# Kernel tuning notes

Hardware: AMD Instinct MI355X
Metric: run time of the kernel (lower is better)

## Reference

```python
import jax, jax.numpy as jnp
import numpy as np
import math

V, D, H, NH, LE, LD = 32000, 256, 1024, 8, 2, 2
B, T = 4, 512


def qlinear(x, W, b):
    # x: [..., Din, 4]; W: [4, Dout, Din] (r,i,j,k); b: [Dout, 4] or None
    r, i, j, k = x[..., 0], x[..., 1], x[..., 2], x[..., 3]
    Wr, Wi, Wj, Wk = W[0], W[1], W[2], W[3]
    f = lambda a, M: jnp.einsum('...d,od->...o', a, M)
    ro = f(r, Wr) - f(i, Wi) - f(j, Wj) - f(k, Wk)
    io = f(r, Wi) + f(i, Wr) + f(j, Wk) - f(k, Wj)
    jo = f(r, Wj) - f(i, Wk) + f(j, Wr) + f(k, Wi)
    ko = f(r, Wk) + f(i, Wj) - f(j, Wi) + f(k, Wr)
    out = jnp.stack([ro, io, jo, ko], axis=-1)
    return out + b if b is not None else out


def modrelu(x, bias):
    # x: [..., F, 4]; bias: [F]
    norm = jnp.linalg.norm(x, axis=-1)
    scale = jax.nn.relu(norm + bias) / (norm + 1e-6)
    return x * scale[..., None]


def qnorm(x, g, beta):
    # normalize each quaternion (last dim of size 4) to unit norm
    n = jnp.sqrt(jnp.sum(x * x, axis=-1, keepdims=True) + 1e-6)
    return g * (x / n) + beta


def qattn(q, k, v, W, b, mask, nh):
    # W: [4(proj q,k,v,out), 4(comp), D, D]; b: [4, D, 4]
    def split(x):
        Bq, Tq, Dq, _ = x.shape
        return x.reshape(Bq, Tq, nh, Dq // nh, 4).transpose(0, 2, 1, 3, 4)
    qh = split(qlinear(q, W[0], b[0]))
    kh = split(qlinear(k, W[1], b[1]))
    vh = split(qlinear(v, W[2], b[2]))
    hd = qh.shape[3]
    s = jnp.einsum('bhqfd,bhkfd->bhqk', qh, kh) / math.sqrt(hd * 4)
    if mask is not None:
        s = jnp.where(mask[:, None] == 0, -jnp.inf, s)
    w = jax.nn.softmax(s, axis=-1)
    o = jnp.einsum('bhqk,bhkfd->bhqfd', w, vh)
    Bq, h, Tq, f, _ = o.shape
    o = o.transpose(0, 2, 1, 3, 4).reshape(Bq, Tq, h * f, 4)
    return qlinear(o, W[3], b[3])


def qff(x, W1, b1, mbias, W2, b2):
    return qlinear(modrelu(qlinear(x, W1, b1), mbias), W2, b2)


def qembed(ids, emb):
    d = emb.shape[-1]
    scale = 1.0 / 10000.0 ** (jnp.arange(d, dtype=jnp.float32) / d)
    r = emb[0][ids]
    i = emb[1][ids] * scale
    j = emb[2][ids] * scale
    k = emb[3][ids] * scale
    n = jnp.sqrt(r * r + i * i + j * j + k * k + 1e-6)
    return jnp.stack([r / n, i / n, j / n, k / n], axis=-1)


def rope(x):
    t, d = x.shape[1], x.shape[2]
    inv = 1.0 / 10000.0 ** (jnp.arange(0, d, 2, dtype=jnp.float32) / d)
    fr = jnp.arange(t, dtype=jnp.float32)[:, None] * inv[None, :]
    ang = jnp.concatenate([jnp.sin(fr), jnp.cos(fr)], axis=-1)  # [T, D]
    return x * ang[None, :, :, None]


def setup_inputs():
    key = jax.random.key(0)
    ks = jax.random.split(key, 12)
    n = lambda k, s: jax.random.normal(k, s, jnp.float32) * 0.02
    src = jax.random.randint(ks[0], (B, T), 0, V)
    tgt = jax.random.randint(ks[1], (B, T), 0, V)
    tgt_mask = jnp.broadcast_to(jnp.tril(jnp.ones((T, T), jnp.int32)), (B, T, T))
    return dict(
        src=src, tgt=tgt, tgt_mask=tgt_mask,
        emb=n(ks[2], (4, V, D)),
        enc_attn_W=n(ks[3], (LE, 4, 4, D, D)), enc_attn_b=jnp.zeros((LE, 4, D, 4)),
        enc_norm_g=jnp.ones((LE, 2, D, 4)), enc_norm_b=jnp.zeros((LE, 2, D, 4)),
        enc_ff_W1=n(ks[4], (LE, 4, H, D)), enc_ff_b1=jnp.zeros((LE, H, 4)),
        enc_ff_mod=jnp.zeros((LE, H)),
        enc_ff_W2=n(ks[5], (LE, 4, D, H)), enc_ff_b2=jnp.zeros((LE, D, 4)),
        dec_sa_W=n(ks[6], (LD, 4, 4, D, D)), dec_sa_b=jnp.zeros((LD, 4, D, 4)),
        dec_ca_W=n(ks[7], (LD, 4, 4, D, D)), dec_ca_b=jnp.zeros((LD, 4, D, 4)),
        dec_norm_g=jnp.ones((LD, 3, D, 4)), dec_norm_b=jnp.zeros((LD, 3, D, 4)),
        dec_ff_W1=n(ks[8], (LD, 4, H, D)), dec_ff_b1=jnp.zeros((LD, H, 4)),
        dec_ff_mod=jnp.zeros((LD, H)),
        dec_ff_W2=n(ks[9], (LD, 4, D, H)), dec_ff_b2=jnp.zeros((LD, D, 4)),
        fc_W=n(ks[10], (V, D)), fc_b=jnp.zeros((V,)),
    )


def reference(src, tgt, tgt_mask, emb,
              enc_attn_W, enc_attn_b, enc_norm_g, enc_norm_b,
              enc_ff_W1, enc_ff_b1, enc_ff_mod, enc_ff_W2, enc_ff_b2,
              dec_sa_W, dec_sa_b, dec_ca_W, dec_ca_b, dec_norm_g, dec_norm_b,
              dec_ff_W1, dec_ff_b1, dec_ff_mod, dec_ff_W2, dec_ff_b2,
              fc_W, fc_b):
    x_src = rope(qembed(src, emb))
    x_tgt = rope(qembed(tgt, emb))
    # encoder stack
    m = x_src
    for l in range(LE):
        m = qnorm(m + qattn(m, m, m, enc_attn_W[l], enc_attn_b[l], None, NH), enc_norm_g[l, 0], enc_norm_b[l, 0])
        m = qnorm(m + qff(m, enc_ff_W1[l], enc_ff_b1[l], enc_ff_mod[l], enc_ff_W2[l], enc_ff_b2[l]), enc_norm_g[l, 1], enc_norm_b[l, 1])
    # decoder stack
    x = x_tgt
    for l in range(LD):
        x = qnorm(x + qattn(x, x, x, dec_sa_W[l], dec_sa_b[l], tgt_mask, NH), dec_norm_g[l, 0], dec_norm_b[l, 0])
        x = qnorm(x + qattn(x, m, m, dec_ca_W[l], dec_ca_b[l], None, NH), dec_norm_g[l, 1], dec_norm_b[l, 1])
        x = qnorm(x + qff(x, dec_ff_W1[l], dec_ff_b1[l], dec_ff_mod[l], dec_ff_W2[l], dec_ff_b2[l]), dec_norm_g[l, 2], dec_norm_b[l, 2])
    real = jnp.linalg.norm(x, axis=-1)  # QuaternionToReal('norm') -> [B, T, D]
    logits = jnp.einsum('btd,vd->btv', real, fc_W) + fc_b
    return logits
```

## Files before the change

### kernel.cpp

```cpp
#include <hip/hip_runtime.h>
#include <math.h>

#define B 4
#define T 512
#define D 256
#define H 1024
#define NH 8
#define V 32000
#define BT (B*T)
#define LE 2
#define LD 2
#define DIM 1024

typedef __attribute__((ext_vector_type(8))) short s16x8;
typedef __attribute__((ext_vector_type(4))) float f32x4;
typedef __attribute__((address_space(3))) void lds_void;
typedef const __attribute__((address_space(1))) void g_void;

__device__ __forceinline__ ushort f2bf(float x) {
  uint u = __float_as_uint(x);
  return (ushort)((u + 0x7fffu + ((u >> 16) & 1u)) >> 16);
}
__device__ __forceinline__ float bf2f(ushort u) {
  return __uint_as_float(((uint)u) << 16);
}

#define QSCALE 0.08838834764831845f

#define A_CNT  1572864
#define F_CNT  2097152
#define FC_CNT 2048000
#define EMB_CNT (2 * BT * 256)
#define MEGA_TOT (A_CNT + F_CNT + FC_CNT + EMB_CNT)
#define WSTEP  1048576
#define FFW    4194304

__device__ __forceinline__ void qexpand_write(
    const float* __restrict__ src, ushort* __restrict__ dst,
    int o, int d, int Din, int P) {
  float w0 = src[(size_t)o * Din + d];
  float w1 = src[P + (size_t)o * Din + d];
  float w2 = src[2 * (size_t)P + (size_t)o * Din + d];
  float w3 = src[3 * (size_t)P + (size_t)o * Din + d];
  int K4 = Din * 4;
  size_t rbase = (size_t)(o * 4) * K4 + d * 4;
  *(ushort4*)(dst + rbase)          = make_ushort4(f2bf(w0), f2bf(-w1), f2bf(-w2), f2bf(-w3));
  *(ushort4*)(dst + rbase + K4)     = make_ushort4(f2bf(w1), f2bf(w0),  f2bf(w3),  f2bf(-w2));
  *(ushort4*)(dst + rbase + 2 * K4) = make_ushort4(f2bf(w2), f2bf(-w3), f2bf(w0),  f2bf(w1));
  *(ushort4*)(dst + rbase + 3 * K4) = make_ushort4(f2bf(w3), f2bf(w2),  f2bf(-w1), f2bf(w0));
}

__global__ __launch_bounds__(256) void mega_expand_kernel(
    const float* __restrict__ encA, const float* __restrict__ decSA,
    const float* __restrict__ decCA,
    const float* __restrict__ eW1, const float* __restrict__ eW2,
    const float* __restrict__ dW1, const float* __restrict__ dW2,
    const float* __restrict__ fcW,
    ushort* __restrict__ WA, ushort* __restrict__ WF, ushort* __restrict__ Wfc,
    const int* __restrict__ srcIds, const int* __restrict__ tgtIds,
    const float* __restrict__ emb,
    float* __restrict__ xsrc, ushort* __restrict__ xbfs,
    float* __restrict__ xtgt, ushort* __restrict__ xbft) {
  int gid = blockIdx.x * 256 + threadIdx.x;
  if (gid < A_CNT) {
    int u = gid >> 18;
    int p = (gid >> 16) & 3;
    int rem = gid & 65535;
    int o = rem >> 8, d = rem & 255;
    const float* base = (u < 2) ? encA + (size_t)u * 1048576
                      : (u < 4) ? decSA + (size_t)(u - 2) * 1048576
                                : decCA + (size_t)(u - 4) * 1048576;
    qexpand_write(base + (size_t)p * 262144,
                  WA + ((size_t)u * 4 + p) * WSTEP, o, d, 256, 65536);
  } else if (gid < A_CNT + F_CNT) {
    int idx = gid - A_CNT;
    int layer = idx >> 19;
    int w12 = (idx >> 18) & 1;
    int rem = idx & 262143;
    const float* w1b = (layer < 2) ? eW1 + (size_t)layer * 1048576
                                   : dW1 + (size_t)(layer - 2) * 1048576;
    const float* w2b = (layer < 2) ? eW2 + (size_t)layer * 1048576
                                   : dW2 + (size_t)(layer - 2) * 1048576;
    ushort* dst = WF + (size_t)layer * 2 * FFW + (size_t)w12 * FFW;
    if (w12 == 0) {
      int o = rem >> 8, d = rem & 255;
      qexpand_write(w1b, dst, o, d, 256, 262144);
    } else {
      int o = rem >> 10, d = rem & 1023;
      qexpand_write(w2b, dst, o, d, 1024, 262144);
    }
  } else if (gid < A_CNT + F_CNT + FC_CNT) {
    int idx = gid - A_CNT - F_CNT;
    float4 v = ((const float4*)fcW)[idx];
    ((ushort4*)Wfc)[idx] = make_ushort4(f2bf(v.x), f2bf(v.y), f2bf(v.z), f2bf(v.w));
  } else if (gid < MEGA_TOT) {
    int idx = gid - A_CNT - F_CNT - FC_CNT;
    int g = idx >> 8, d = idx & 255;
    int isTgt = g >= BT;
    int bt = isTgt ? g - BT : g;
    int id = isTgt ? tgtIds[bt] : srcIds[bt];
    float* out = isTgt ? xtgt : xsrc;
    ushort* outbf = isTgt ? xbft : xbfs;
    int t = bt % T;
    size_t VD = (size_t)V * D;
    float scale = powf(10000.f, -(float)d / (float)D);
    float r = emb[(size_t)id * D + d];
    float i = emb[VD + (size_t)id * D + d] * scale;
    float j = emb[2 * VD + (size_t)id * D + d] * scale;
    float k = emb[3 * VD + (size_t)id * D + d] * scale;
    float n = sqrtf(r * r + i * i + j * j + k * k + 1e-6f);
    float ang;
    if (d < D / 2) {
      float inv = powf(10000.f, -(float)(2 * d) / (float)D);
      ang = sinf((float)t * inv);
    } else {
      float inv = powf(10000.f, -(float)(2 * (d - D / 2)) / (float)D);
      ang = cosf((float)t * inv);
    }
    float s = ang / n;
    size_t base = (size_t)bt * DIM + d * 4;
    float4 q = make_float4(r * s, i * s, j * s, k * s);
    *(float4*)(out + base) = q;
    *(ushort4*)(outbf + base) = make_ushort4(f2bf(q.x), f2bf(q.y), f2bf(q.z), f2bf(q.w));
  }
}

struct GP {
  const ushort* A; const ushort* Aalt; int altStart;
  const ushort* Bt; const float* bias; void* Cv;
  ushort* qo; ushort* ko; ushort* vo;
  const float* modb;
};

template <int OMODE, int TM>
__global__ __launch_bounds__(256, 4) void gemm_bf16_kernel(
    GP u0, GP u1, int nunits, int nsplit, int N, int K) {
  __shared__ ushort As[2][TM * 32];
  __shared__ ushort Bs[2][128 * 32];
  const int tid = threadIdx.x;
  const int w = tid >> 6, l = tid & 63;
  const int nwg = gridDim.x;
  const int qq = nwg >> 3, rr = nwg & 7;
  const int xcd = blockIdx.x & 7, pos = blockIdx.x >> 3;
  const int wg = (xcd < rr ? xcd * (qq + 1) : rr * (qq + 1) + (xcd - rr) * qq) + pos;
  const int uwg = nwg / (nunits * nsplit);
  const int idx = wg / uwg;
  const int unit = idx / nsplit;
  const int split = idx % nsplit;
  const int wgl = wg % uwg;
  GP U = unit ? u1 : u0;
  const int Ksub = K / nsplit;
  const int kbase = split * Ksub;
  const int nbx = N >> 7;
  const int nby = uwg / nbx;
  const int m0 = (wgl % nby) * TM, n0 = (wgl / nby) * 128;
  const ushort* Ap = (U.altStart && n0 >= U.altStart) ? U.Aalt : U.A;
  const ushort* Btp = U.Bt;
  const int lr = l & 15, lg = l >> 4;
  constexpr int NR = (TM == 128) ? 4 : 2;
  const int wm = (TM == 128) ? (w >> 1) : 0;
  const int wn = (TM == 128) ? (w & 1) : w;
  const int wcol = wn * (NR * 16);
  f32x4 acc[4][NR] = {};
  const int NT = Ksub >> 5;

  auto stage = [&](int t, int buf) {
    int k0 = kbase + (t << 5);
#pragma unroll
    for (int s = 0; s < TM / 64; ++s) {
      int fb = (w * (TM / 64) + s) * 1024;
      int f = fb + l * 16;
      int row = f >> 6, cb = (f & 63) >> 1;
      __builtin_amdgcn_global_load_lds(
          (g_void*)(Ap + (size_t)(m0 + row) * K + k0 + cb),
          (lds_void*)((char*)&As[buf][0] + fb), 16, 0, 0);
    }
#pragma unroll
    for (int s = 0; s < 2; ++s) {
      int fb = (w * 2 + s) * 1024;
      int f = fb + l * 16;
      int row = f >> 6, cb = (f & 63) >> 1;
      __builtin_amdgcn_global_load_lds(
          (g_void*)(Btp + (size_t)(n0 + row) * K + k0 + cb),
          (lds_void*)((char*)&Bs[buf][0] + fb), 16, 0, 0);
    }
  };
  auto compute = [&](int buf) {
    s16x8 af[4], bfr[NR];
#pragma unroll
    for (int mi = 0; mi < 4; ++mi)
      af[mi] = *(const s16x8*)(&As[buf][0] + (wm * 64 + mi * 16 + lr) * 32 + lg * 8);
#pragma unroll
    for (int ni = 0; ni < NR; ++ni)
      bfr[ni] = *(const s16x8*)(&Bs[buf][0] + (wcol + ni * 16 + lr) * 32 + lg * 8);
    __builtin_amdgcn_s_setprio(1);
#pragma unroll
    for (int mi = 0; mi < 4; ++mi)
#pragma unroll
      for (int ni = 0; ni < NR; ++ni)
        acc[mi][ni] = __builtin_amdgcn_mfma_f32_16x16x32_bf16(af[mi], bfr[ni], acc[mi][ni], 0, 0, 0);
    __builtin_amdgcn_s_setprio(0);
  };

  stage(0, 0);
  __syncthreads();
  int cur = 0;
  for (int t = 0; t < NT; ++t) {
    if (t + 1 < NT) stage(t + 1, cur ^ 1);
    compute(cur);
    __syncthreads();
    cur ^= 1;
  }

#pragma unroll
  for (int mi = 0; mi < 4; ++mi) {
#pragma unroll
    for (int ni = 0; ni < NR; ++ni) {
      int row = m0 + wm * 64 + mi * 16 + lg * 4;
      int col = n0 + wcol + ni * 16 + lr;
      f32x4 v = acc[mi][ni];
      if constexpr (OMODE == 0) {
        float bv = U.bias ? U.bias[col] : 0.f;
        float* C = (float*)U.Cv;
#pragma unroll
        for (int r = 0; r < 4; ++r)
          C[(size_t)(row + r) * N + col] = v[r] + bv;
      } else if constexpr (OMODE == 3) {
        float bv = U.bias[col];
        if (col < 2048) {
          ushort* dst = (col < DIM) ? U.qo : U.ko;
          float sc = (col < DIM) ? QSCALE : 1.f;
          int c = col & (DIM - 1);
#pragma unroll
          for (int r = 0; r < 4; ++r)
            dst[(size_t)(row + r) * DIM + c] = f2bf((v[r] + bv) * sc);
        } else {
          int c = col - 2048;
          ushort4 o4 = make_ushort4(f2bf(v[0] + bv), f2bf(v[1] + bv),
                                    f2bf(v[2] + bv), f2bf(v[3] + bv));
          *(ushort4*)&U.vo[((size_t)((row >> 9) << 10) + c) * T + (row & 511)] = o4;
        }
      } else if constexpr (OMODE == 5) {
        float bv = U.bias[col];
        float mb = U.modb[col >> 2];
        ushort* C = (ushort*)U.Cv;
#pragma unroll
        for (int r = 0; r < 4; ++r) {
          float val = v[r] + bv;
          float sq = val * val;
          sq += __shfl_xor(sq, 1);
          sq += __shfl_xor(sq, 2);
          float norm = sqrtf(sq);
          float scale = fmaxf(norm + mb, 0.f) / (norm + 1e-6f);
          C[(size_t)(row + r) * N + col] = f2bf(val * scale);
        }
      } else {
        ushort* P = (ushort*)U.Cv + (size_t)split * BT * N;
#pragma unroll
        for (int r = 0; r < 4; ++r)
          P[(size_t)(row + r) * N + col] = f2bf(v[r]);
      }
    }
  }
}

struct MP {
  const ushort* P; const float* bias;
  float* xres; ushort* xbf;
  const float* gg; const float* bb; ushort* realo;
};

__global__ __launch_bounds__(256) void merge_qnorm_kernel(MP m0, MP m1) {
  int blk = blockIdx.x;
  MP M = (blk >= BT) ? m1 : m0;
  int row = (blk >= BT) ? blk - BT : blk;
  int c4 = threadIdx.x << 2;
  size_t base = (size_t)row * DIM + c4;
  float a0 = 0.f, a1 = 0.f, a2 = 0.f, a3 = 0.f;
#pragma unroll
  for (int sp = 0; sp < 4; ++sp) {
    ushort4 p = *(const ushort4*)(M.P + (size_t)sp * BT * DIM + base);
    a0 += bf2f(p.x); a1 += bf2f(p.y); a2 += bf2f(p.z); a3 += bf2f(p.w);
  }
  float4 xv = *(float4*)(M.xres + base);
  float v0 = a0 + M.bias[c4 + 0] + xv.x;
  float v1 = a1 + M.bias[c4 + 1] + xv.y;
  float v2 = a2 + M.bias[c4 + 2] + xv.z;
  float v3 = a3 + M.bias[c4 + 3] + xv.w;
  float invn = rsqrtf(v0 * v0 + v1 * v1 + v2 * v2 + v3 * v3 + 1e-6f);
  float r0 = M.gg[c4 + 0] * (v0 * invn) + M.bb[c4 + 0];
  float r1 = M.gg[c4 + 1] * (v1 * invn) + M.bb[c4 + 1];
  float r2 = M.gg[c4 + 2] * (v2 * invn) + M.bb[c4 + 2];
  float r3 = M.gg[c4 + 3] * (v3 * invn) + M.bb[c4 + 3];
  *(float4*)(M.xres + base) = make_float4(r0, r1, r2, r3);
  *(ushort4*)(M.xbf + base) = make_ushort4(f2bf(r0), f2bf(r1), f2bf(r2), f2bf(r3));
  if (M.realo)
    M.realo[(size_t)row * D + (c4 >> 2)] =
        f2bf(sqrtf(r0 * r0 + r1 * r1 + r2 * r2 + r3 * r3));
}

__global__ __launch_bounds__(256) void fused_attn_kernel(
    const ushort* __restrict__ qb, const ushort* __restrict__ kb,
    const ushort* __restrict__ vT, ushort* __restrict__ outA,
    int c0, int c1) {
  __shared__ ushort Ks[2][64 * 128];
  __shared__ ushort Vs[2][128 * 64];
  __shared__ ushort Pst[4][1024];
  const int tid = threadIdx.x;
  const int wq = tid >> 6, l = tid & 63;
  const int lr = l & 15, lg = l >> 4;
  const int h = blockIdx.y;
  const int u = blockIdx.z >> 2, b = blockIdx.z & 3;
  const size_t uoff = (size_t)u * ((size_t)BT * DIM);
  const int causal = u ? c1 : c0;
  const int q0 = blockIdx.x * 64 + wq * 16;
  const size_t bT = (size_t)b * T;
  const int hc = h * 128;
  const size_t vrow0 = (size_t)(b * NH + h) * 128;
  const ushort* qbu = qb + uoff;
  const ushort* kbu = kb + uoff;
  const ushort* vTu = vT + uoff;
  ushort* outu = outA + uoff;
  s16x8 qf[4];
#pragma unroll
  for (int ks = 0; ks < 4; ++ks)
    qf[ks] = *(const s16x8*)(qbu + (bT + q0 + lr) * DIM + hc + ks * 32 + lg * 8);
  f32x4 O[8] = {};
  float m[4] = {-3e38f, -3e38f, -3e38f, -3e38f};
  float lac[4] = {0.f, 0.f, 0.f, 0.f};
  const int kend = causal ? (blockIdx.x + 1) * 64 : T;
  const int ntile = kend >> 6;

  auto stageKV = [&](int tile, int buf) {
    int kv0 = tile << 6;
#pragma unroll
    for (int s = 0; s < 4; ++s) {
      int f = s * 4096 + tid * 16;
      int row = f >> 8, g = (f >> 4) & 15;
      int gs = g ^ (row & 7);
      __builtin_amdgcn_global_load_lds(
          (g_void*)(kbu + (bT + kv0 + row) * DIM + hc + gs * 8),
          (lds_void*)((char*)&Ks[buf][0] + f), 16, 0, 0);
    }
#pragma unroll
    for (int s = 0; s < 4; ++s) {
      int f = s * 4096 + tid * 16;
      int row = f >> 7, g = (f >> 4) & 7;
      int gs = g ^ (row & 7);
      __builtin_amdgcn_global_load_lds(
          (g_void*)(vTu + (vrow0 + row) * T + kv0 + gs * 8),
          (lds_void*)((char*)&Vs[buf][0] + f), 16, 0, 0);
    }
  };

  stageKV(0, 0);
  __syncthreads();
  int cur = 0;
  for (int tile = 0; tile < ntile; ++tile) {
    const int kv0 = tile << 6;
    if (tile + 1 < ntile) stageKV(tile + 1, cur ^ 1);
    f32x4 s[4] = {};
#pragma unroll
    for (int ks = 0; ks < 4; ++ks) {
      s16x8 kf[4];
#pragma unroll
      for (int ni = 0; ni < 4; ++ni) {
        int row = ni * 16 + lr;
        int g = (ks * 4 + lg) ^ (row & 7);
        kf[ni] = *(const s16x8*)(&Ks[cur][0] + row * 128 + g * 8);
      }
#pragma unroll
      for (int ni = 0; ni < 4; ++ni)
        s[ni] = __builtin_amdgcn_mfma_f32_16x16x32_bf16(qf[ks], kf[ni], s[ni], 0, 0, 0);
    }
    const bool domask = causal && (kv0 + 63 > q0);
#pragma unroll
    for (int r = 0; r < 4; ++r) {
      const int qrow = q0 + lg * 4 + r;
      float mx = -3e38f;
#pragma unroll
      for (int ni = 0; ni < 4; ++ni) {
        float v = s[ni][r];
        if (domask && (kv0 + ni * 16 + lr > qrow)) v = -3e38f;
        s[ni][r] = v;
        mx = fmaxf(mx, v);
      }
#pragma unroll
      for (int dd = 1; dd < 16; dd <<= 1) mx = fmaxf(mx, __shfl_xor(mx, dd));
      if (__ballot(mx > m[r] + 8.f)) {
        float mn = fmaxf(m[r], mx);
        float alpha = __expf(m[r] - mn);
        m[r] = mn;
        lac[r] *= alpha;
#pragma unroll
        for (int dni = 0; dni < 8; ++dni) O[dni][r] *= alpha;
      }
      float ps = 0.f;
#pragma unroll
      for (int ni = 0; ni < 4; ++ni) {
        float p = __expf(s[ni][r] - m[r]);
        s[ni][r] = p;
        ps += p;
      }
#pragma unroll
      for (int dd = 1; dd < 16; dd <<= 1) ps += __shfl_xor(ps, dd);
      lac[r] += ps;
      const int qloc = lg * 4 + r;
      const int sw = (qloc & 7) << 3;
#pragma unroll
      for (int ni = 0; ni < 4; ++ni)
        Pst[wq][qloc * 64 + ((ni * 16 + lr) ^ sw)] = f2bf(s[ni][r]);
    }
    asm volatile("s_waitcnt lgkmcnt(0)" ::: "memory");
    __builtin_amdgcn_sched_barrier(0);
#pragma unroll
    for (int ks2 = 0; ks2 < 2; ++ks2) {
      s16x8 pa = *(const s16x8*)&Pst[wq][lr * 64 + ((ks2 * 32 + lg * 8) ^ ((lr & 7) << 3))];
#pragma unroll
      for (int dni = 0; dni < 8; ++dni) {
        int row = dni * 16 + lr;
        int g = (ks2 * 4 + lg) ^ (row & 7);
        s16x8 vf = *(const s16x8*)(&Vs[cur][0] + row * 64 + g * 8);
        O[dni] = __builtin_amdgcn_mfma_f32_16x16x32_bf16(pa, vf, O[dni], 0, 0, 0);
      }
    }
    __syncthreads();
    cur ^= 1;
  }
#pragma unroll
  for (int r = 0; r < 4; ++r) {
    float inv = 1.f / lac[r];
    const size_t row = bT + q0 + lg * 4 + r;
#pragma unroll
    for (int dni = 0; dni < 8; ++dni)
      outu[row * DIM + hc + dni * 16 + lr] = f2bf(O[dni][r] * inv);
  }
}

extern "C" void kernel_launch(void* const* d_in, const int* in_sizes, int n_in,
                              void* d_out, int out_size, void* d_ws, size_t ws_size,
                              hipStream_t stream) {
  const int*   src        = (const int*)d_in[0];
  const int*   tgt        = (const int*)d_in[1];
  const float* emb        = (const float*)d_in[3];
  const float* enc_attn_W = (const float*)d_in[4];
  const float* enc_attn_b = (const float*)d_in[5];
  const float* enc_norm_g = (const float*)d_in[6];
  const float* enc_norm_b = (const float*)d_in[7];
  const float* enc_ff_W1  = (const float*)d_in[8];
  const float* enc_ff_b1  = (const float*)d_in[9];
  const float* enc_ff_mod = (const float*)d_in[10];
  const float* enc_ff_W2  = (const float*)d_in[11];
  const float* enc_ff_b2  = (const float*)d_in[12];
  const float* dec_sa_W   = (const float*)d_in[13];
  const float* dec_sa_b   = (const float*)d_in[14];
  const float* dec_ca_W   = (const float*)d_in[15];
  const float* dec_ca_b   = (const float*)d_in[16];
  const float* dec_norm_g = (const float*)d_in[17];
  const float* dec_norm_b = (const float*)d_in[18];
  const float* dec_ff_W1  = (const float*)d_in[19];
  const float* dec_ff_b1  = (const float*)d_in[20];
  const float* dec_ff_mod = (const float*)d_in[21];
  const float* dec_ff_W2  = (const float*)d_in[22];
  const float* dec_ff_b2  = (const float*)d_in[23];
  const float* fc_W       = (const float*)d_in[24];
  const float* fc_b       = (const float*)d_in[25];
  float* out = (float*)d_out;

  const size_t USZ = (size_t)BT * DIM;
  float* ws    = (float*)d_ws;
  float* xsrc  = ws;
  float* xtgt  = xsrc + USZ;
  ushort* xbf_src = (ushort*)(xtgt + USZ);
  ushort* xbf_tgt = xbf_src + USZ;
  ushort* aobf    = xbf_tgt + USZ;
  ushort* qb      = aobf + 2 * USZ;
  ushort* kb      = qb + 2 * USZ;
  ushort* vTb     = kb + 2 * USZ;
  ushort* hbf     = vTb + 2 * USZ;
  ushort* realbf  = hbf + (size_t)BT * H * 4;
  ushort* WA      = realbf + (size_t)BT * D;
  ushort* WF      = WA + (size_t)6 * 4 * WSTEP;
  ushort* Wfc     = WF + (size_t)4 * 2 * FFW;
  ushort* Pff     = Wfc + (size_t)V * D;

  mega_expand_kernel<<<(MEGA_TOT + 255) / 256, 256, 0, stream>>>(
      enc_attn_W, dec_sa_W, dec_ca_W,
      enc_ff_W1, enc_ff_W2, dec_ff_W1, dec_ff_W2, fc_W, WA, WF, Wfc,
      src, tgt, emb, xsrc, xbf_src, xtgt, xbf_tgt);

  GP Z{};
  MP MZ{};

  auto mkQKV = [&](const ushort* Abf, const ushort* Wu, const float* bb, int u) {
    GP g = Z;
    g.A = Abf; g.Bt = Wu; g.bias = bb;
    g.qo = qb + u * USZ; g.ko = kb + u * USZ; g.vo = vTb + u * USZ;
    return g;
  };
  auto mkMP = [&](const ushort* P, const float* bb, float* xres, ushort* xbf,
                  const float* gg, const float* nb, ushort* realo) {
    MP m = MZ;
    m.P = P; m.bias = bb; m.xres = xres; m.xbf = xbf;
    m.gg = gg; m.bb = nb; m.realo = realo;
    return m;
  };

  auto qkv1 = [&](GP g) {
    gemm_bf16_kernel<3, 128><<<384, 256, 0, stream>>>(g, g, 1, 1, 3 * DIM, DIM);
  };
  auto qkv2 = [&](GP g0, GP g1) {
    gemm_bf16_kernel<3, 128><<<768, 256, 0, stream>>>(g0, g1, 2, 1, 3 * DIM, DIM);
  };
  auto op1 = [&](int u, const ushort* Wu3, MP m) {
    GP g = Z;
    g.A = aobf + u * USZ; g.Bt = Wu3; g.Cv = Pff;
    gemm_bf16_kernel<6, 64><<<1024, 256, 0, stream>>>(g, g, 1, 4, DIM, DIM);
    merge_qnorm_kernel<<<BT, 256, 0, stream>>>(m, m);
  };
  auto op2 = [&](const ushort* We3, const ushort* Wd3, MP me, MP md) {
    GP g0 = Z, g1 = Z;
    g0.A = aobf; g0.Bt = We3; g0.Cv = Pff;
    g1.A = aobf + USZ; g1.Bt = Wd3; g1.Cv = Pff + 4 * USZ;
    gemm_bf16_kernel<6, 64><<<2048, 256, 0, stream>>>(g0, g1, 2, 4, DIM, DIM);
    merge_qnorm_kernel<<<2 * BT, 256, 0, stream>>>(me, md);
  };
  auto attn1 = [&](int causal) {
    fused_attn_kernel<<<dim3(T / 64, NH, B), 256, 0, stream>>>(
        qb, kb, vTb, aobf, causal, causal);
  };
  auto ffpair = [&](const ushort* xbf, int layer, const float* b1,
                    const float* mod, const float* b2, float* xres,
                    ushort* xbfo, const float* gg, const float* nb,
                    ushort* realo) {
    const ushort* Wf = WF + (size_t)layer * 2 * FFW;
    GP g1 = Z;
    g1.A = xbf; g1.Bt = Wf; g1.bias = b1; g1.Cv = hbf; g1.modb = mod;
    gemm_bf16_kernel<5, 128><<<512, 256, 0, stream>>>(g1, g1, 1, 1, 4 * H, DIM);
    GP g2 = Z;
    g2.A = hbf; g2.Bt = Wf + FFW; g2.Cv = Pff;
    gemm_bf16_kernel<6, 64><<<1024, 256, 0, stream>>>(g2, g2, 1, 4, DIM, 4 * H);
    MP m = mkMP(Pff, b2, xres, xbfo, gg, nb, realo);
    merge_qnorm_kernel<<<BT, 256, 0, stream>>>(m, m);
  };

  {
    GP e = mkQKV(xbf_src, WA + (size_t)(0 * 4) * WSTEP, enc_attn_b, 0);
    GP d = mkQKV(xbf_tgt, WA + (size_t)(2 * 4) * WSTEP, dec_sa_b, 1);
    qkv2(e, d);
    fused_attn_kernel<<<dim3(T / 64, NH, 2 * B), 256, 0, stream>>>(
        qb, kb, vTb, aobf, 0, 1);
    MP me = mkMP(Pff, enc_attn_b + 3 * DIM, xsrc, xbf_src,
                 enc_norm_g, enc_norm_b, nullptr);
    MP md = mkMP(Pff + 4 * USZ, dec_sa_b + 3 * DIM, xtgt, xbf_tgt,
                 dec_norm_g, dec_norm_b, nullptr);
    op2(WA + (size_t)(0 * 4 + 3) * WSTEP, WA + (size_t)(2 * 4 + 3) * WSTEP, me, md);
  }
  ffpair(xbf_src, 0, enc_ff_b1, enc_ff_mod, enc_ff_b2, xsrc, xbf_src,
         enc_norm_g + 1 * DIM, enc_norm_b + 1 * DIM, nullptr);
  {
    GP e = mkQKV(xbf_src, WA + (size_t)(1 * 4) * WSTEP,
                 enc_attn_b + (size_t)1 * 4 * DIM, 0);
    qkv1(e);
    attn1(0);
    MP me = mkMP(Pff, enc_attn_b + (size_t)1 * 4 * DIM + 3 * DIM, xsrc, xbf_src,
                 enc_norm_g + 2 * DIM, enc_norm_b + 2 * DIM, nullptr);
    op1(0, WA + (size_t)(1 * 4 + 3) * WSTEP, me);
  }
  ffpair(xbf_src, 1, enc_ff_b1 + (size_t)1 * H * 4, enc_ff_mod + H,
         enc_ff_b2 + DIM, xsrc, xbf_src,
         enc_norm_g + 3 * DIM, enc_norm_b + 3 * DIM, nullptr);

  for (int l = 0; l < LD; ++l) {
    if (l > 0) {
      GP d = mkQKV(xbf_tgt, WA + (size_t)((2 + l) * 4) * WSTEP,
                   dec_sa_b + (size_t)l * 4 * DIM, 0);
      qkv1(d);
      attn1(1);
      MP md = mkMP(Pff, dec_sa_b + (size_t)l * 4 * DIM + 3 * DIM, xtgt, xbf_tgt,
                   dec_norm_g + (size_t)(l * 3) * DIM,
                   dec_norm_b + (size_t)(l * 3) * DIM, nullptr);
      op1(0, WA + (size_t)((2 + l) * 4 + 3) * WSTEP, md);
    }
    {
      GP g = mkQKV(xbf_tgt, WA + (size_t)((4 + l) * 4) * WSTEP,
                   dec_ca_b + (size_t)l * 4 * DIM, 0);
      g.Aalt = xbf_src; g.altStart = DIM;
      qkv1(g);
      attn1(0);
      MP mg = mkMP(Pff, dec_ca_b + (size_t)l * 4 * DIM + 3 * DIM, xtgt, xbf_tgt,
                   dec_norm_g + (size_t)(l * 3 + 1) * DIM,
                   dec_norm_b + (size_t)(l * 3 + 1) * DIM, nullptr);
      op1(0, WA + (size_t)((4 + l) * 4 + 3) * WSTEP, mg);
    }
    ffpair(xbf_tgt, 2 + l, dec_ff_b1 + (size_t)l * H * 4,
           dec_ff_mod + (size_t)l * H, dec_ff_b2 + (size_t)l * DIM,
           xtgt, xbf_tgt, dec_norm_g + (size_t)(l * 3 + 2) * DIM,
           dec_norm_b + (size_t)(l * 3 + 2) * DIM,
           (l == LD - 1) ? realbf : nullptr);
  }

  {
    GP g = Z;
    g.A = realbf; g.Bt = Wfc; g.bias = fc_b; g.Cv = out;
    gemm_bf16_kernel<0, 128><<<(V / 128) * (BT / 128), 256, 0, stream>>>(
        g, g, 1, 1, V, 256);
  }
}
```

Before: 930.3 us.

## Fuse split-K reduction and qnorm into GEMM via last-arriving-block counter

Removes the separate merge_qnorm kernel launches after each split-K output GEMM. Each workgroup bumps a per-tile atomic counter after writing its partial, and the fourth (last) arriver sums the four bf16 partials and applies bias, residual, quaternion norm, and optional real-norm output for its tile. This saves a kernel launch and a round of scheduling per residual block, at the cost of threadfences, an atomic per tile, and serialized tail work in the last workgroup.

```diff
diff --git a/kernel.cpp b/kernel.cpp
--- a/kernel.cpp
+++ b/kernel.cpp
@@ -130,6 +130,8 @@
   const ushort* Bt; const float* bias; void* Cv;
   ushort* qo; ushort* ko; ushort* vo;
   const float* modb;
+  float* xres; ushort* xbf; const float* gg; const float* bb; ushort* realo;
+  uint* ctr;
 };
 
 template <int OMODE, int TM>
@@ -262,41 +264,48 @@
       }
     }
   }
-}
-
-struct MP {
-  const ushort* P; const float* bias;
-  float* xres; ushort* xbf;
-  const float* gg; const float* bb; ushort* realo;
-};
-
-__global__ __launch_bounds__(256) void merge_qnorm_kernel(MP m0, MP m1) {
-  int blk = blockIdx.x;
-  MP M = (blk >= BT) ? m1 : m0;
-  int row = (blk >= BT) ? blk - BT : blk;
-  int c4 = threadIdx.x << 2;
-  size_t base = (size_t)row * DIM + c4;
-  float a0 = 0.f, a1 = 0.f, a2 = 0.f, a3 = 0.f;
-#pragma unroll
-  for (int sp = 0; sp < 4; ++sp) {
-    ushort4 p = *(const ushort4*)(M.P + (size_t)sp * BT * DIM + base);
-    a0 += bf2f(p.x); a1 += bf2f(p.y); a2 += bf2f(p.z); a3 += bf2f(p.w);
-  }
-  float4 xv = *(float4*)(M.xres + base);
-  float v0 = a0 + M.bias[c4 + 0] + xv.x;
-  float v1 = a1 + M.bias[c4 + 1] + xv.y;
-  float v2 = a2 + M.bias[c4 + 2] + xv.z;
-  float v3 = a3 + M.bias[c4 + 3] + xv.w;
-  float invn = rsqrtf(v0 * v0 + v1 * v1 + v2 * v2 + v3 * v3 + 1e-6f);
-  float r0 = M.gg[c4 + 0] * (v0 * invn) + M.bb[c4 + 0];
-  float r1 = M.gg[c4 + 1] * (v1 * invn) + M.bb[c4 + 1];
-  float r2 = M.gg[c4 + 2] * (v2 * invn) + M.bb[c4 + 2];
-  float r3 = M.gg[c4 + 3] * (v3 * invn) + M.bb[c4 + 3];
-  *(float4*)(M.xres + base) = make_float4(r0, r1, r2, r3);
-  *(ushort4*)(M.xbf + base) = make_ushort4(f2bf(r0), f2bf(r1), f2bf(r2), f2bf(r3));
-  if (M.realo)
-    M.realo[(size_t)row * D + (c4 >> 2)] =
-        f2bf(sqrtf(r0 * r0 + r1 * r1 + r2 * r2 + r3 * r3));
+
+  if constexpr (OMODE == 6) {
+    __threadfence();
+    __syncthreads();
+    __shared__ uint sOld;
+    if (tid == 0) sOld = atomicAdd(U.ctr + wgl, 1u);
+    __syncthreads();
+    if (sOld == 3u) {
+      __threadfence();
+      const ushort* Pb = (const ushort*)U.Cv;
+#pragma unroll
+      for (int it = 0; it < 8; ++it) {
+        int q = it * 256 + tid;
+        int rrow = m0 + (q >> 5);
+        int c4 = n0 + ((q & 31) << 2);
+        size_t base = (size_t)rrow * DIM + c4;
+        float a0 = 0.f, a1 = 0.f, a2 = 0.f, a3 = 0.f;
+#pragma unroll
+        for (int sp = 0; sp < 4; ++sp) {
+          ushort4 p = *(const ushort4*)(Pb + (size_t)sp * BT * DIM + base);
+          a0 += bf2f(p.x); a1 += bf2f(p.y); a2 += bf2f(p.z); a3 += bf2f(p.w);
+        }
+        float4 xv = *(float4*)(U.xres + base);
+        float v0 = a0 + U.bias[c4 + 0] + xv.x;
+        float v1 = a1 + U.bias[c4 + 1] + xv.y;
+        float v2 = a2 + U.bias[c4 + 2] + xv.z;
+        float v3 = a3 + U.bias[c4 + 3] + xv.w;
+        float invn = rsqrtf(v0 * v0 + v1 * v1 + v2 * v2 + v3 * v3 + 1e-6f);
+        float r0 = U.gg[c4 + 0] * (v0 * invn) + U.bb[c4 + 0];
+        float r1 = U.gg[c4 + 1] * (v1 * invn) + U.bb[c4 + 1];
+        float r2 = U.gg[c4 + 2] * (v2 * invn) + U.bb[c4 + 2];
+        float r3 = U.gg[c4 + 3] * (v3 * invn) + U.bb[c4 + 3];
+        *(float4*)(U.xres + base) = make_float4(r0, r1, r2, r3);
+        *(ushort4*)(U.xbf + base) =
+            make_ushort4(f2bf(r0), f2bf(r1), f2bf(r2), f2bf(r3));
+        if (U.realo)
+          U.realo[(size_t)rrow * D + (c4 >> 2)] =
+              f2bf(sqrtf(r0 * r0 + r1 * r1 + r2 * r2 + r3 * r3));
+      }
+      if (tid == 0) atomicExch(U.ctr + wgl, 0u);
+    }
+  }
 }
 
 __global__ __launch_bounds__(256) void fused_attn_kernel(
@@ -483,6 +492,9 @@
   ushort* WF      = WA + (size_t)6 * 4 * WSTEP;
   ushort* Wfc     = WF + (size_t)4 * 2 * FFW;
   ushort* Pff     = Wfc + (size_t)V * D;
+  uint*   Pctr    = (uint*)(Pff + 8 * USZ);
+
+  hipMemsetAsync(Pctr, 0, 512 * sizeof(uint), stream);
 
   mega_expand_kernel<<<(MEGA_TOT + 255) / 256, 256, 0, stream>>>(
       enc_attn_W, dec_sa_W, dec_ca_W,
@@ -490,7 +502,6 @@
       src, tgt, emb, xsrc, xbf_src, xtgt, xbf_tgt);
 
   GP Z{};
-  MP MZ{};
 
   auto mkQKV = [&](const ushort* Abf, const ushort* Wu, const float* bb, int u) {
     GP g = Z;
@@ -498,12 +509,13 @@
     g.qo = qb + u * USZ; g.ko = kb + u * USZ; g.vo = vTb + u * USZ;
     return g;
   };
-  auto mkMP = [&](const ushort* P, const float* bb, float* xres, ushort* xbf,
-                  const float* gg, const float* nb, ushort* realo) {
-    MP m = MZ;
-    m.P = P; m.bias = bb; m.xres = xres; m.xbf = xbf;
-    m.gg = gg; m.bb = nb; m.realo = realo;
-    return m;
+  auto mkSK = [&](const ushort* Abf, const ushort* Wt, ushort* Pbuf, uint* ctr,
+                  const float* bb, float* xres, ushort* xbf, const float* gg,
+                  const float* nb, ushort* realo) {
+    GP g = Z;
+    g.A = Abf; g.Bt = Wt; g.Cv = Pbuf; g.ctr = ctr; g.bias = bb;
+    g.xres = xres; g.xbf = xbf; g.gg = gg; g.bb = nb; g.realo = realo;
+    return g;
   };
 
   auto qkv1 = [&](GP g) {
@@ -511,23 +523,15 @@
   };
   auto qkv2 = [&](GP g0, GP g1) {
     gemm_bf16_kernel<3, 128><<<768, 256, 0, stream>>>(g0, g1, 2, 1, 3 * DIM, DIM);
-  };
-  auto op1 = [&](int u, const ushort* Wu3, MP m) {
-    GP g = Z;
-    g.A = aobf + u * USZ; g.Bt = Wu3; g.Cv = Pff;
-    gemm_bf16_kernel<6, 64><<<1024, 256, 0, stream>>>(g, g, 1, 4, DIM, DIM);
-    merge_qnorm_kernel<<<BT, 256, 0, stream>>>(m, m);
-  };
-  auto op2 = [&](const ushort* We3, const ushort* Wd3, MP me, MP md) {
-    GP g0 = Z, g1 = Z;
-    g0.A = aobf; g0.Bt = We3; g0.Cv = Pff;
-    g1.A = aobf + USZ; g1.Bt = Wd3; g1.Cv = Pff + 4 * USZ;
-    gemm_bf16_kernel<6, 64><<<2048, 256, 0, stream>>>(g0, g1, 2, 4, DIM, DIM);
-    merge_qnorm_kernel<<<2 * BT, 256, 0, stream>>>(me, md);
   };
   auto attn1 = [&](int causal) {
     fused_attn_kernel<<<dim3(T / 64, NH, B), 256, 0, stream>>>(
         qb, kb, vTb, aobf, causal, causal);
+  };
+  auto op1 = [&](int u, const ushort* Wu3, const float* bb, float* xres,
+                 ushort* xbf, const float* gg, const float* nb) {
+    GP g = mkSK(aobf + u * USZ, Wu3, Pff, Pctr, bb, xres, xbf, gg, nb, nullptr);
+    gemm_bf16_kernel<6, 64><<<1024, 256, 0, stream>>>(g, g, 1, 4, DIM, DIM);
   };
   auto ffpair = [&](const ushort* xbf, int layer, const float* b1,
                     const float* mod, const float* b2, float* xres,
@@ -537,11 +541,8 @@
     GP g1 = Z;
     g1.A = xbf; g1.Bt = Wf; g1.bias = b1; g1.Cv = hbf; g1.modb = mod;
     gemm_bf16_kernel<5, 128><<<512, 256, 0, stream>>>(g1, g1, 1, 1, 4 * H, DIM);
-    GP g2 = Z;
-    g2.A = hbf; g2.Bt = Wf + FFW; g2.Cv = Pff;
+    GP g2 = mkSK(hbf, Wf + FFW, Pff, Pctr, b2, xres, xbfo, gg, nb, realo);
     gemm_bf16_kernel<6, 64><<<1024, 256, 0, stream>>>(g2, g2, 1, 4, DIM, 4 * H);
-    MP m = mkMP(Pff, b2, xres, xbfo, gg, nb, realo);
-    merge_qnorm_kernel<<<BT, 256, 0, stream>>>(m, m);
   };
 
   {
@@ -550,11 +551,13 @@
     qkv2(e, d);
     fused_attn_kernel<<<dim3(T / 64, NH, 2 * B), 256, 0, stream>>>(
         qb, kb, vTb, aobf, 0, 1);
-    MP me = mkMP(Pff, enc_attn_b + 3 * DIM, xsrc, xbf_src,
-                 enc_norm_g, enc_norm_b, nullptr);
-    MP md = mkMP(Pff + 4 * USZ, dec_sa_b + 3 * DIM, xtgt, xbf_tgt,
-                 dec_norm_g, dec_norm_b, nullptr);
-    op2(WA + (size_t)(0 * 4 + 3) * WSTEP, WA + (size_t)(2 * 4 + 3) * WSTEP, me, md);
+    GP eo = mkSK(aobf, WA + (size_t)(0 * 4 + 3) * WSTEP, Pff, Pctr,
+                 enc_attn_b + 3 * DIM, xsrc, xbf_src, enc_norm_g, enc_norm_b,
+                 nullptr);
+    GP dd = mkSK(aobf + USZ, WA + (size_t)(2 * 4 + 3) * WSTEP, Pff + 4 * USZ,
+                 Pctr + 256, dec_sa_b + 3 * DIM, xtgt, xbf_tgt, dec_norm_g,
+                 dec_norm_b, nullptr);
+    gemm_bf16_kernel<6, 64><<<2048, 256, 0, stream>>>(eo, dd, 2, 4, DIM, DIM);
   }
   ffpair(xbf_src, 0, enc_ff_b1, enc_ff_mod, enc_ff_b2, xsrc, xbf_src,
          enc_norm_g + 1 * DIM, enc_norm_b + 1 * DIM, nullptr);
@@ -563,9 +566,9 @@
                  enc_attn_b + (size_t)1 * 4 * DIM, 0);
     qkv1(e);
     attn1(0);
-    MP me = mkMP(Pff, enc_attn_b + (size_t)1 * 4 * DIM + 3 * DIM, xsrc, xbf_src,
-                 enc_norm_g + 2 * DIM, enc_norm_b + 2 * DIM, nullptr);
-    op1(0, WA + (size_t)(1 * 4 + 3) * WSTEP, me);
+    op1(0, WA + (size_t)(1 * 4 + 3) * WSTEP,
+        enc_attn_b + (size_t)1 * 4 * DIM + 3 * DIM, xsrc, xbf_src,
+        enc_norm_g + 2 * DIM, enc_norm_b + 2 * DIM);
   }
   ffpair(xbf_src, 1, enc_ff_b1 + (size_t)1 * H * 4, enc_ff_mod + H,
          enc_ff_b2 + DIM, xsrc, xbf_src,
@@ -577,10 +580,10 @@
                    dec_sa_b + (size_t)l * 4 * DIM, 0);
       qkv1(d);
       attn1(1);
-      MP md = mkMP(Pff, dec_sa_b + (size_t)l * 4 * DIM + 3 * DIM, xtgt, xbf_tgt,
-                   dec_norm_g + (size_t)(l * 3) * DIM,
-                   dec_norm_b + (size_t)(l * 3) * DIM, nullptr);
-      op1(0, WA + (size_t)((2 + l) * 4 + 3) * WSTEP, md);
+      op1(0, WA + (size_t)((2 + l) * 4 + 3) * WSTEP,
+          dec_sa_b + (size_t)l * 4 * DIM + 3 * DIM, xtgt, xbf_tgt,
+          dec_norm_g + (size_t)(l * 3) * DIM,
+          dec_norm_b + (size_t)(l * 3) * DIM);
     }
     {
       GP g = mkQKV(xbf_tgt, WA + (size_t)((4 + l) * 4) * WSTEP,
@@ -588,10 +591,10 @@
       g.Aalt = xbf_src; g.altStart = DIM;
       qkv1(g);
       attn1(0);
-      MP mg = mkMP(Pff, dec_ca_b + (size_t)l * 4 * DIM + 3 * DIM, xtgt, xbf_tgt,
-                   dec_norm_g + (size_t)(l * 3 + 1) * DIM,
-                   dec_norm_b + (size_t)(l * 3 + 1) * DIM, nullptr);
-      op1(0, WA + (size_t)((4 + l) * 4 + 3) * WSTEP, mg);
+      op1(0, WA + (size_t)((4 + l) * 4 + 3) * WSTEP,
+          dec_ca_b + (size_t)l * 4 * DIM + 3 * DIM, xtgt, xbf_tgt,
+          dec_norm_g + (size_t)(l * 3 + 1) * DIM,
+          dec_norm_b + (size_t)(l * 3 + 1) * DIM);
     }
     ffpair(xbf_tgt, 2 + l, dec_ff_b1 + (size_t)l * H * 4,
            dec_ff_mod + (size_t)l * H, dec_ff_b2 + (size_t)l * DIM,
```

Result: slower. 3.033 ms (+226.0%).
